# Performance work log

Hardware: AMD Instinct MI355X
Metric: run time of the kernel (lower is better)

The kernel has to match this reference:

```python
import jax, jax.numpy as jnp
import numpy as np

WD, WH, WW = 2, 7, 7
N = WD * WH * WW            # 98 tokens per window
C = 192                     # dim
H = 6                       # num_heads
HD = C // H                 # head_dim = 32
NW = 512                    # number of windows per sample
B = 4                       # batch
B_ = B * NW                 # 2048 windows total
TABLE = (2 * WD - 1) * (2 * WH - 1) * (2 * WW - 1)  # 507


def _relative_position_index():
    d, h, w = np.meshgrid(np.arange(WD), np.arange(WH), np.arange(WW), indexing='ij')
    coords = np.stack([d, h, w]).reshape(3, -1)              # (3, N)
    rel = coords[:, :, None] - coords[:, None, :]            # (3, N, N)
    rel = rel.transpose(1, 2, 0).astype(np.int64)            # (N, N, 3)
    rel[:, :, 0] += WD - 1
    rel[:, :, 1] += WH - 1
    rel[:, :, 2] += WW - 1
    rel[:, :, 0] *= (2 * WH - 1) * (2 * WW - 1)
    rel[:, :, 1] *= 2 * WW - 1
    return jnp.asarray(rel.sum(-1), dtype=jnp.int32)         # (N, N)


def setup_inputs() -> dict:
    key = jax.random.key(0)
    ks = jax.random.split(key, 7)
    return {
        'x': jax.random.normal(ks[0], (B_, N, C), dtype=jnp.float32),
        'mask': jax.random.normal(ks[1], (NW, N, N), dtype=jnp.float32),
        'qkv_w': jax.random.normal(ks[2], (3 * C, C), dtype=jnp.float32) * 0.02,
        'qkv_b': jnp.zeros((3 * C,), dtype=jnp.float32),
        'proj_w': jax.random.normal(ks[3], (C, C), dtype=jnp.float32) * 0.02,
        'proj_b': jnp.zeros((C,), dtype=jnp.float32),
        'rpb_table': jax.random.normal(ks[4], (TABLE, H), dtype=jnp.float32) * 0.02,
        'rel_pos_index': _relative_position_index(),
    }


def reference(x, mask, qkv_w, qkv_b, proj_w, proj_b, rpb_table, rel_pos_index):
    Bw, n, c = x.shape
    hd = c // H
    scale = hd ** -0.5
    qkv = (x @ qkv_w.T + qkv_b).reshape(Bw, n, 3, H, hd)
    q, k, v = qkv[:, :, 0], qkv[:, :, 1], qkv[:, :, 2]       # (Bw, n, H, hd)
    # attn = (q @ k^T) * scale  (scale applied after matmul, as in source)
    attn = jnp.einsum('bihd,bjhd->bhij', q, k) * scale       # (Bw, H, n, n)
    bias = rpb_table[rel_pos_index]                          # (n, n, H)
    attn = attn + jnp.transpose(bias, (2, 0, 1))[None]       # broadcast over Bw
    nw = mask.shape[0]
    attn = attn.reshape(Bw // nw, nw, H, n, n) + mask[None, :, None]
    attn = jax.nn.softmax(attn.reshape(Bw, H, n, n), axis=-1)
    out = jnp.einsum('bhij,bjhd->bihd', attn, v).reshape(Bw, n, c)
    return out @ proj_w.T + proj_b
```

## Files before the change

kernel.cpp:

```cpp
#include <hip/hip_runtime.h>
#include <hip/hip_bf16.h>

using bf16   = __bf16;
using bf16x4 = __attribute__((ext_vector_type(4))) __bf16;
using bf16x8 = __attribute__((ext_vector_type(8))) __bf16;
using f32x4  = __attribute__((ext_vector_type(4))) float;

#define B_TOT 2048
#define NTOK  98
#define CDIM  192
#define NHEAD 6
#define HDIM  32
#define NWIN  512
#define NN    (NTOK*NTOK)
#define QKV_ELEMS ((size_t)B_TOT*NHEAD*NTOK*HDIM)
#define MROWS 200704
#define SCALE 0.17677669529663687f

#define MFMA(a,b,c) __builtin_amdgcn_mfma_f32_16x16x32_bf16((a),(b),(c),0,0,0)

#define GLD16(gp, lp) __builtin_amdgcn_global_load_lds(                        \
    (const __attribute__((address_space(1))) void*)(gp),                       \
    (__attribute__((address_space(3))) void*)(lp), 16, 0, 0)

__global__ void build_bias(const float* __restrict__ table,
                           const int* __restrict__ rel,
                           float* __restrict__ bias) {
    int t = blockIdx.x * 256 + threadIdx.x;
    if (t < NN) {
        int idx = rel[t];
        #pragma unroll
        for (int h = 0; h < NHEAD; ++h)
            bias[h * NN + t] = table[idx * NHEAD + h];
    }
}

__global__ void conv_swz(const float* __restrict__ src, bf16* __restrict__ dst,
                         int nchunk) {
    int t = blockIdx.x * 256 + threadIdx.x;
    if (t < nchunk) {
        int row = t / 24, c = t % 24;
        const float* s = src + (size_t)row * CDIM + c * 8;
        bf16x8 o;
        #pragma unroll
        for (int e = 0; e < 8; ++e) o[e] = (bf16)s[e];
        *(bf16x8*)(dst + (size_t)row * CDIM + ((c ^ (row & 7)) << 3)) = o;
    }
}

__global__ __launch_bounds__(256) void qkv_gemm(
    const float* __restrict__ x, const bf16* __restrict__ wb,
    const float* __restrict__ bvec,
    bf16* __restrict__ qdst, bf16* __restrict__ kdst, bf16* __restrict__ vdst)
{
    __shared__ char Bs[2][24576];
    const int tid = threadIdx.x, lane = tid & 63, wv = tid >> 6;
    const int l15 = lane & 15, l16 = lane >> 4;
    const int m0 = blockIdx.x * 64;

    {
        const char* bsrc = (const char*)wb;
        #pragma unroll
        for (int j = 0; j < 6; ++j) {
            const int ch = wv * 6 + j;
            GLD16(bsrc + ch * 1024 + lane * 16, Bs[0] + ch * 1024);
        }
    }

    const int arow = wv * 16 + l15;
    const int grow = m0 + arow;
    const float* xr = x + (size_t)grow * CDIM + l16 * 8;
    bf16x8 af[6];
    #pragma unroll
    for (int ks = 0; ks < 6; ++ks) {
        float4 v0 = *(const float4*)(xr + ks * 32);
        float4 v1 = *(const float4*)(xr + ks * 32 + 4);
        bf16x8 a;
        a[0] = (bf16)v0.x; a[1] = (bf16)v0.y; a[2] = (bf16)v0.z; a[3] = (bf16)v0.w;
        a[4] = (bf16)v1.x; a[5] = (bf16)v1.y; a[6] = (bf16)v1.z; a[7] = (bf16)v1.w;
        af[ks] = a;
    }

    __syncthreads();

    const int rowoff = (grow / NTOK) * 18816 + (grow % NTOK) * 32;
    const f32x4 z4 = {0.f, 0.f, 0.f, 0.f};

    #pragma unroll
    for (int nc = 0; nc < 9; ++nc) {
        if (nc < 8) {
            const char* bsrc = (const char*)wb + (size_t)(nc + 1) * 24576;
            #pragma unroll
            for (int j = 0; j < 6; ++j) {
                const int ch = wv * 6 + j;
                GLD16(bsrc + ch * 1024 + lane * 16, Bs[(nc + 1) & 1] + ch * 1024);
            }
        }

        f32x4 acc[4];
        #pragma unroll
        for (int ct = 0; ct < 4; ++ct) acc[ct] = z4;

        #pragma unroll
        for (int ks = 0; ks < 6; ++ks) {
            #pragma unroll
            for (int ct = 0; ct < 4; ++ct) {
                const int brow = ct * 16 + l15;
                bf16x8 bf = *(const bf16x8*)(Bs[nc & 1] + brow * 384
                                             + (((ks * 4 + l16) ^ (brow & 7)) << 4));
                acc[ct] = MFMA(bf, af[ks], acc[ct]);
            }
        }

        #pragma unroll
        for (int ct = 0; ct < 4; ++ct) {
            const int g0    = nc * 64 + ct * 16;
            const int which = g0 / CDIM;
            const int cm    = g0 % CDIM;
            const int h     = cm >> 5, hd0 = cm & 31;
            const float4 bvf = *(const float4*)(bvec + g0 + l16 * 4);
            bf16x4 s;
            #pragma unroll
            for (int r = 0; r < 4; ++r) {
                float v = acc[ct][r] + ((const float*)&bvf)[r];
                if (which == 0) v *= SCALE;
                s[r] = (bf16)v;
            }
            bf16* dp = (which == 0) ? qdst : (which == 1) ? kdst : vdst;
            *(bf16x4*)(dp + rowoff + h * 3136 + hd0 + l16 * 4) = s;
        }
        __syncthreads();
    }
}

__global__ __launch_bounds__(256) void attn_fused(
    const bf16* __restrict__ q, const bf16* __restrict__ k,
    const bf16* __restrict__ v,
    const float* __restrict__ mask, const float* __restrict__ bias,
    bf16* __restrict__ ao)
{
    __shared__ char lds[4 * 8192 + 4 * 4096 + 4 * 64];
    const int tid = threadIdx.x, lane = tid & 63, wv = tid >> 6;
    const int l15 = lane & 15, l16 = lane >> 4;
    char*  Vt   = lds + wv * 8192;
    char*  P    = lds + 32768 + wv * 4096;
    float* invS = (float*)(lds + 49152 + wv * 64);

    const int u = blockIdx.x * 4 + wv;
    const int b = u / NHEAD, h = u - b * NHEAD;
    const int w = b & (NWIN - 1);
    const size_t bho = (size_t)u * 3136;

    bf16x8 vvv[7];
    #pragma unroll
    for (int t = 0; t < 7; ++t) {
        int idx = t * 64 + lane;
        int n = idx >> 2; if (n > 97) n = 97;
        int hd0 = (idx & 3) * 8;
        vvv[t] = *(const bf16x8*)(v + bho + n * 32 + hd0);
    }

    bf16x8 kf[7];
    #pragma unroll
    for (int jt = 0; jt < 7; ++jt) {
        int kr = jt * 16 + l15; if (kr > 97) kr = 97;
        kf[jt] = *(const bf16x8*)(k + bho + kr * HDIM + l16 * 8);
    }

    #pragma unroll
    for (int t = 0; t < 7; ++t) {
        int idx = t * 64 + lane;
        if (idx < 392) {
            int n = idx >> 2, hd0 = (idx & 3) * 8;
            #pragma unroll
            for (int e = 0; e < 8; ++e) {
                int hd = hd0 + e;
                *(bf16*)(Vt + hd * 256 + (((n >> 3) ^ (hd & 7)) << 4) + ((n & 7) << 1))
                    = vvv[t][e];
            }
        }
    }
    #pragma unroll
    for (int t = 0; t < 15; ++t) {
        int idx = t * 64 + lane;
        int hd = idx / 30, n = 98 + idx % 30;
        *(bf16*)(Vt + hd * 256 + (((n >> 3) ^ (hd & 7)) << 4) + ((n & 7) << 1)) = (bf16)0.f;
    }
    {
        int zr = lane >> 2;
        int zc = 112 + (lane & 3) * 4;
        *(unsigned long long*)(P + zr * 256 + (((zc >> 3) ^ (zr & 7)) << 4)
                               + ((zc & 7) << 1)) = 0ull;
    }

    const float* mrow = mask + (size_t)w * NN;
    const float* brow = bias + (size_t)h * NN;
    bf16* dst = ao + (size_t)b * NTOK * CDIM;
    const f32x4 z4 = {0.f, 0.f, 0.f, 0.f};

    #pragma unroll 1
    for (int it = 0; it < 7; ++it) {
        int qrow = it * 16 + l15; if (qrow > 97) qrow = 97;
        const bf16x8 qf = *(const bf16x8*)(q + bho + qrow * HDIM + l16 * 8);
        f32x4 acc[7];
        #pragma unroll
        for (int jt = 0; jt < 7; ++jt)
            acc[jt] = MFMA(qf, kf[jt], z4);

        #pragma unroll
        for (int r = 0; r < 4; ++r) {
            int i = it * 16 + l16 * 4 + r; if (i > 97) i = 97;
            float s = 0.f;
            #pragma unroll
            for (int jt = 0; jt < 7; ++jt) {
                int j = jt * 16 + l15;
                float mbv = (j < NTOK) ? (mrow[i * NTOK + j] + brow[i * NTOK + j])
                                       : -__builtin_inff();
                float e = __expf(acc[jt][r] + mbv);
                acc[jt][r] = e; s += e;
            }
            s += __shfl_xor(s, 1, 16);
            s += __shfl_xor(s, 2, 16);
            s += __shfl_xor(s, 4, 16);
            s += __shfl_xor(s, 8, 16);
            if (l15 == 0) invS[l16 * 4 + r] = 1.f / s;
        }

        #pragma unroll
        for (int jt = 0; jt < 7; ++jt) {
            #pragma unroll
            for (int r = 0; r < 4; ++r) {
                int row = l16 * 4 + r;
                int j = jt * 16 + l15;
                *(bf16*)(P + row * 256 + (((j >> 3) ^ (row & 7)) << 4) + ((j & 7) << 1))
                    = (bf16)acc[jt][r];
            }
        }

        f32x4 o0 = z4, o1 = z4;
        #pragma unroll
        for (int ks = 0; ks < 4; ++ks) {
            int kchunk = ks * 4 + l16;
            bf16x8 pf = *(const bf16x8*)(P + l15 * 256 + ((kchunk ^ (l15 & 7)) << 4));
            bf16x8 v0 = *(const bf16x8*)(Vt + l15 * 256 + ((kchunk ^ (l15 & 7)) << 4));
            bf16x8 v1 = *(const bf16x8*)(Vt + (16 + l15) * 256 + ((kchunk ^ (l15 & 7)) << 4));
            o0 = MFMA(v0, pf, o0);
            o1 = MFMA(v1, pf, o1);
        }

        {
            int row = it * 16 + l15;
            if (row < NTOK) {
                float inv = invS[l15];
                bf16x4 s0, s1;
                #pragma unroll
                for (int r = 0; r < 4; ++r) {
                    s0[r] = (bf16)(o0[r] * inv);
                    s1[r] = (bf16)(o1[r] * inv);
                }
                const int swr = (b * NTOK + row) & 7;
                const int c0 = h * 4 + (l16 >> 1);
                const int c1 = c0 + 2;
                const int wi = (l16 & 1) << 2;
                *(bf16x4*)(dst + (size_t)row * CDIM + (((c0 ^ swr) << 3) | wi)) = s0;
                *(bf16x4*)(dst + (size_t)row * CDIM + (((c1 ^ swr) << 3) | wi)) = s1;
            }
        }
    }
}

__global__ __launch_bounds__(256) void proj_gemm(
    const bf16* __restrict__ ao, const bf16* __restrict__ wb,
    const float* __restrict__ bvec, float* __restrict__ out)
{
    __shared__ char As[24576];
    __shared__ char Bs[2][24576];
    const int tid = threadIdx.x, lane = tid & 63, wv = tid >> 6;
    const int l15 = lane & 15, l16 = lane >> 4;
    const int m0 = blockIdx.x * 64;

    {
        const char* asrc = (const char*)ao + (size_t)m0 * 384;
        const char* bsrc = (const char*)wb;
        #pragma unroll
        for (int j = 0; j < 6; ++j) {
            const int ch = wv * 6 + j;
            GLD16(asrc + ch * 1024 + lane * 16, As + ch * 1024);
            GLD16(bsrc + ch * 1024 + lane * 16, Bs[0] + ch * 1024);
        }
    }
    __syncthreads();

    const int arow = wv * 16 + l15;
    bf16x8 af[6];
    #pragma unroll
    for (int ks = 0; ks < 6; ++ks)
        af[ks] = *(const bf16x8*)(As + arow * 384 + (((ks * 4 + l16) ^ (arow & 7)) << 4));

    const size_t orow = (size_t)(m0 + arow) * CDIM;
    const f32x4 z4 = {0.f, 0.f, 0.f, 0.f};

    #pragma unroll
    for (int nc = 0; nc < 3; ++nc) {
        if (nc < 2) {
            const char* bsrc = (const char*)wb + (size_t)(nc + 1) * 24576;
            #pragma unroll
            for (int j = 0; j < 6; ++j) {
                const int ch = wv * 6 + j;
                GLD16(bsrc + ch * 1024 + lane * 16, Bs[(nc + 1) & 1] + ch * 1024);
            }
        }

        f32x4 acc[4];
        #pragma unroll
        for (int ct = 0; ct < 4; ++ct) acc[ct] = z4;

        #pragma unroll
        for (int ks = 0; ks < 6; ++ks) {
            #pragma unroll
            for (int ct = 0; ct < 4; ++ct) {
                const int brow = ct * 16 + l15;
                bf16x8 bf = *(const bf16x8*)(Bs[nc & 1] + brow * 384
                                             + (((ks * 4 + l16) ^ (brow & 7)) << 4));
                acc[ct] = MFMA(bf, af[ks], acc[ct]);
            }
        }

        #pragma unroll
        for (int ct = 0; ct < 4; ++ct) {
            const int g0 = nc * 64 + ct * 16;
            const float4 bvf = *(const float4*)(bvec + g0 + l16 * 4);
            f32x4 s;
            #pragma unroll
            for (int r = 0; r < 4; ++r)
                s[r] = acc[ct][r] + ((const float*)&bvf)[r];
            *(f32x4*)(out + orow + g0 + l16 * 4) = s;
        }
        __syncthreads();
    }
}

extern "C" void kernel_launch(void* const* d_in, const int* in_sizes, int n_in,
                              void* d_out, int out_size, void* d_ws, size_t ws_size,
                              hipStream_t stream)
{
    (void)in_sizes; (void)n_in; (void)out_size; (void)ws_size;
    const float* x      = (const float*)d_in[0];
    const float* mask   = (const float*)d_in[1];
    const float* qkv_w  = (const float*)d_in[2];
    const float* qkv_b  = (const float*)d_in[3];
    const float* proj_w = (const float*)d_in[4];
    const float* proj_b = (const float*)d_in[5];
    const float* rpb    = (const float*)d_in[6];
    const int*   rel    = (const int*)d_in[7];
    float* out = (float*)d_out;

    char* ws = (char*)d_ws;
    bf16* qb = (bf16*)ws;
    bf16* kb = qb + QKV_ELEMS;
    bf16* vb = kb + QKV_ELEMS;
    size_t off = 3 * QKV_ELEMS * sizeof(bf16);
    float* bias = (float*)(ws + off);
    off += ((size_t)NHEAD * NN * 4 + 255) / 256 * 256;
    bf16* ao = (bf16*)(ws + off);
    bf16* qwb = ao;
    bf16* pwb = qb;

    build_bias<<<(NN + 255) / 256, 256, 0, stream>>>(rpb, rel, bias);
    conv_swz<<<(576 * 24 + 255) / 256, 256, 0, stream>>>(qkv_w, qwb, 576 * 24);
    qkv_gemm<<<MROWS / 64, 256, 0, stream>>>(x, qwb, qkv_b, qb, kb, vb);
    attn_fused<<<(B_TOT * NHEAD) / 4, 256, 0, stream>>>(qb, kb, vb, mask, bias, ao);
    conv_swz<<<(192 * 24 + 255) / 256, 256, 0, stream>>>(proj_w, pwb, 192 * 24);
    proj_gemm<<<MROWS / 64, 256, 0, stream>>>(ao, pwb, proj_b, out);
}
```

Before: 335.2 us.

## Store V pre-transposed in global memory and read MFMA operands directly

The QKV GEMM now writes V transposed per (window, head) into a padded buffer of hd×112, placed in the output buffer as scratch, with a new kernel zeroing the padding columns. The attention kernel drops the per-wave LDS transpose of V and the matching LDS allocation, and loads V fragments straight from global memory for the PV MFMA. This removes LDS scatter traffic and lowers LDS use, which may allow higher occupancy. In exchange, V stores in the GEMM become strided 2-byte scatters and the PV loop issues uncoalesced global loads.

```diff
diff --git a/kernel.cpp b/kernel.cpp
--- a/kernel.cpp
+++ b/kernel.cpp
@@ -14,6 +14,9 @@
 #define NWIN  512
 #define NN    (NTOK*NTOK)
 #define QKV_ELEMS ((size_t)B_TOT*NHEAD*NTOK*HDIM)
+#define NUNIT (B_TOT*NHEAD)
+#define VSTRIDE 112
+#define VUNIT  (HDIM*VSTRIDE)
 #define MROWS 200704
 #define SCALE 0.17677669529663687f
 
@@ -32,6 +35,15 @@
         #pragma unroll
         for (int h = 0; h < NHEAD; ++h)
             bias[h * NN + t] = table[idx * NHEAD + h];
+    }
+}
+
+__global__ void zero_vpad(bf16* __restrict__ vT) {
+    int t = blockIdx.x * 256 + threadIdx.x;
+    int total = NUNIT * HDIM * 7;
+    for (; t < total; t += 2688 * 256) {
+        int row = t / 7, d = t % 7;
+        *(unsigned*)((char*)vT + (size_t)row * (VSTRIDE * 2) + 196 + d * 4) = 0u;
     }
 }
 
@@ -51,7 +63,7 @@
 __global__ __launch_bounds__(256) void qkv_gemm(
     const float* __restrict__ x, const bf16* __restrict__ wb,
     const float* __restrict__ bvec,
-    bf16* __restrict__ qdst, bf16* __restrict__ kdst, bf16* __restrict__ vdst)
+    bf16* __restrict__ qdst, bf16* __restrict__ kdst, bf16* __restrict__ vT)
 {
     __shared__ char Bs[2][24576];
     const int tid = threadIdx.x, lane = tid & 63, wv = tid >> 6;
@@ -83,7 +95,8 @@
 
     __syncthreads();
 
-    const int rowoff = (grow / NTOK) * 18816 + (grow % NTOK) * 32;
+    const int gb = grow / NTOK, gn = grow % NTOK;
+    const int rowoff = gb * 18816 + gn * 32;
     const f32x4 z4 = {0.f, 0.f, 0.f, 0.f};
 
     #pragma unroll
@@ -119,15 +132,23 @@
             const int cm    = g0 % CDIM;
             const int h     = cm >> 5, hd0 = cm & 31;
             const float4 bvf = *(const float4*)(bvec + g0 + l16 * 4);
-            bf16x4 s;
-            #pragma unroll
-            for (int r = 0; r < 4; ++r) {
-                float v = acc[ct][r] + ((const float*)&bvf)[r];
-                if (which == 0) v *= SCALE;
-                s[r] = (bf16)v;
-            }
-            bf16* dp = (which == 0) ? qdst : (which == 1) ? kdst : vdst;
-            *(bf16x4*)(dp + rowoff + h * 3136 + hd0 + l16 * 4) = s;
+            if (which == 2) {
+                bf16* vp = vT + (size_t)(gb * NHEAD + h) * VUNIT
+                         + (hd0 + l16 * 4) * VSTRIDE + gn;
+                #pragma unroll
+                for (int r = 0; r < 4; ++r)
+                    vp[r * VSTRIDE] = (bf16)(acc[ct][r] + ((const float*)&bvf)[r]);
+            } else {
+                bf16x4 s;
+                #pragma unroll
+                for (int r = 0; r < 4; ++r) {
+                    float v = acc[ct][r] + ((const float*)&bvf)[r];
+                    if (which == 0) v *= SCALE;
+                    s[r] = (bf16)v;
+                }
+                bf16* dp = (which == 0) ? qdst : kdst;
+                *(bf16x4*)(dp + rowoff + h * 3136 + hd0 + l16 * 4) = s;
+            }
         }
         __syncthreads();
     }
@@ -135,30 +156,21 @@
 
 __global__ __launch_bounds__(256) void attn_fused(
     const bf16* __restrict__ q, const bf16* __restrict__ k,
-    const bf16* __restrict__ v,
+    const bf16* __restrict__ vT,
     const float* __restrict__ mask, const float* __restrict__ bias,
     bf16* __restrict__ ao)
 {
-    __shared__ char lds[4 * 8192 + 4 * 4096 + 4 * 64];
+    __shared__ char lds[4 * 4096 + 4 * 64];
     const int tid = threadIdx.x, lane = tid & 63, wv = tid >> 6;
     const int l15 = lane & 15, l16 = lane >> 4;
-    char*  Vt   = lds + wv * 8192;
-    char*  P    = lds + 32768 + wv * 4096;
-    float* invS = (float*)(lds + 49152 + wv * 64);
+    char*  P    = lds + wv * 4096;
+    float* invS = (float*)(lds + 16384 + wv * 64);
 
     const int u = blockIdx.x * 4 + wv;
     const int b = u / NHEAD, h = u - b * NHEAD;
     const int w = b & (NWIN - 1);
     const size_t bho = (size_t)u * 3136;
-
-    bf16x8 vvv[7];
-    #pragma unroll
-    for (int t = 0; t < 7; ++t) {
-        int idx = t * 64 + lane;
-        int n = idx >> 2; if (n > 97) n = 97;
-        int hd0 = (idx & 3) * 8;
-        vvv[t] = *(const bf16x8*)(v + bho + n * 32 + hd0);
-    }
+    const bf16* vu = vT + (size_t)u * VUNIT;
 
     bf16x8 kf[7];
     #pragma unroll
@@ -167,25 +179,6 @@
         kf[jt] = *(const bf16x8*)(k + bho + kr * HDIM + l16 * 8);
     }
 
-    #pragma unroll
-    for (int t = 0; t < 7; ++t) {
-        int idx = t * 64 + lane;
-        if (idx < 392) {
-            int n = idx >> 2, hd0 = (idx & 3) * 8;
-            #pragma unroll
-            for (int e = 0; e < 8; ++e) {
-                int hd = hd0 + e;
-                *(bf16*)(Vt + hd * 256 + (((n >> 3) ^ (hd & 7)) << 4) + ((n & 7) << 1))
-                    = vvv[t][e];
-            }
-        }
-    }
-    #pragma unroll
-    for (int t = 0; t < 15; ++t) {
-        int idx = t * 64 + lane;
-        int hd = idx / 30, n = 98 + idx % 30;
-        *(bf16*)(Vt + hd * 256 + (((n >> 3) ^ (hd & 7)) << 4) + ((n & 7) << 1)) = (bf16)0.f;
-    }
     {
         int zr = lane >> 2;
         int zc = 112 + (lane & 3) * 4;
@@ -242,8 +235,8 @@
         for (int ks = 0; ks < 4; ++ks) {
             int kchunk = ks * 4 + l16;
             bf16x8 pf = *(const bf16x8*)(P + l15 * 256 + ((kchunk ^ (l15 & 7)) << 4));
-            bf16x8 v0 = *(const bf16x8*)(Vt + l15 * 256 + ((kchunk ^ (l15 & 7)) << 4));
-            bf16x8 v1 = *(const bf16x8*)(Vt + (16 + l15) * 256 + ((kchunk ^ (l15 & 7)) << 4));
+            bf16x8 v0 = *(const bf16x8*)(vu + l15 * VSTRIDE + ks * 32 + l16 * 8);
+            bf16x8 v1 = *(const bf16x8*)(vu + (16 + l15) * VSTRIDE + ks * 32 + l16 * 8);
             o0 = MFMA(v0, pf, o0);
             o1 = MFMA(v1, pf, o1);
         }
@@ -358,18 +351,19 @@
     char* ws = (char*)d_ws;
     bf16* qb = (bf16*)ws;
     bf16* kb = qb + QKV_ELEMS;
-    bf16* vb = kb + QKV_ELEMS;
-    size_t off = 3 * QKV_ELEMS * sizeof(bf16);
+    size_t off = 2 * QKV_ELEMS * sizeof(bf16);
     float* bias = (float*)(ws + off);
     off += ((size_t)NHEAD * NN * 4 + 255) / 256 * 256;
     bf16* ao = (bf16*)(ws + off);
+    bf16* vT  = (bf16*)d_out;
     bf16* qwb = ao;
     bf16* pwb = qb;
 
+    zero_vpad<<<2688, 256, 0, stream>>>(vT);
     build_bias<<<(NN + 255) / 256, 256, 0, stream>>>(rpb, rel, bias);
     conv_swz<<<(576 * 24 + 255) / 256, 256, 0, stream>>>(qkv_w, qwb, 576 * 24);
-    qkv_gemm<<<MROWS / 64, 256, 0, stream>>>(x, qwb, qkv_b, qb, kb, vb);
-    attn_fused<<<(B_TOT * NHEAD) / 4, 256, 0, stream>>>(qb, kb, vb, mask, bias, ao);
+    qkv_gemm<<<MROWS / 64, 256, 0, stream>>>(x, qwb, qkv_b, qb, kb, vT);
+    attn_fused<<<NUNIT / 4, 256, 0, stream>>>(qb, kb, vT, mask, bias, ao);
     conv_swz<<<(192 * 24 + 255) / 256, 256, 0, stream>>>(proj_w, pwb, 192 * 24);
     proj_gemm<<<MROWS / 64, 256, 0, stream>>>(ao, pwb, proj_b, out);
 }
```

New measurement: 378.3 us. 12.9% more time.
